# Kernel tuning notes

Hardware: AMD Instinct MI355X
Metric: run time of the kernel (lower is better)

Reference implementation:

```python
import jax, jax.numpy as jnp
import numpy as np

N_WIRES = 8
DIM = 1 << N_WIRES  # 256

# Precompute CNOT permutations (torchquantum convention: wire 0 = MSB)
_idx = np.arange(DIM)
_CNOT_PERMS = []
for _c in range(N_WIRES):
    _t = (_c + 1) % N_WIRES
    _cbit = (_idx >> (N_WIRES - 1 - _c)) & 1
    _CNOT_PERMS.append(np.where(_cbit == 1, _idx ^ (1 << (N_WIRES - 1 - _t)), _idx))
# PauliZ signs per wire: [DIM, N_WIRES]
_ZSIGNS = np.stack([1.0 - 2.0 * ((_idx >> (N_WIRES - 1 - w)) & 1) for w in range(N_WIRES)], axis=1).astype(np.float32)


def _quantum_heads(x, theta):
    """x: [B,S,H,8] angles; theta: [8]. Returns PauliZ expectations [B,S,H,8].

    Simulates per (token,head) an 8-qubit circuit: RX(x_i+theta_i) on wire i
    (encoder RX followed by trainable RX on same wire = one RX with summed angle),
    then CNOT ring 0->1..6->7, 7->0, then MeasureAll PauliZ.
    """
    B, S, H, _ = x.shape
    N = B * S * H
    ang = x.reshape(N, N_WIRES) + theta  # [N,8]
    state = jnp.zeros((N, DIM), dtype=jnp.complex64).at[:, 0].set(1.0)
    half = ang * 0.5
    c_all = jnp.cos(half)
    s_all = jnp.sin(half)
    for w in range(N_WIRES):
        A = 1 << w
        Bdim = 1 << (N_WIRES - 1 - w)
        s = state.reshape(N, A, 2, Bdim)
        a0, a1 = s[:, :, 0, :], s[:, :, 1, :]
        c = c_all[:, w][:, None, None].astype(jnp.complex64)
        isn = (1j * s_all[:, w][:, None, None]).astype(jnp.complex64)
        n0 = c * a0 - isn * a1
        n1 = -isn * a0 + c * a1
        state = jnp.stack([n0, n1], axis=2).reshape(N, DIM)
    for perm in _CNOT_PERMS:
        state = state[:, perm]
    probs = state.real ** 2 + state.imag ** 2  # [N,256]
    exp = probs @ jnp.asarray(_ZSIGNS)  # [N,8]
    return exp.reshape(B, S, H, N_WIRES)


def _mha(proj, W_combine, num_heads):
    # proj: [B,S,E]; q = k = v = proj (identical deterministic projections)
    B, S, E = proj.shape
    d_k = E // num_heads
    qkv = proj.reshape(B, S, num_heads, d_k).transpose(0, 2, 1, 3)  # [B,H,S,dk]
    scores = jnp.einsum('bhqd,bhkd->bhqk', qkv, qkv) / jnp.sqrt(jnp.float32(d_k))
    attn = jax.nn.softmax(scores, axis=-1)
    out = jnp.einsum('bhqk,bhkd->bhqd', attn, qkv)
    out = out.transpose(0, 2, 1, 3).reshape(B, S, E)
    return out @ W_combine.T


def setup_inputs() -> dict:
    key = jax.random.key(0)
    k1, k2, k3 = jax.random.split(key, 3)
    B, S, H = 8, 1024, 8
    E = H * N_WIRES  # 64
    x = jax.random.normal(k1, (B, S, E), dtype=jnp.float32)
    theta = jax.random.normal(k2, (N_WIRES,), dtype=jnp.float32)
    W_combine = jax.random.normal(k3, (E, E), dtype=jnp.float32) * (1.0 / np.sqrt(E))
    return {'x': x, 'theta': theta, 'W_combine': W_combine}


def reference(x, theta, W_combine):
    B, S, E = x.shape
    H = E // N_WIRES
    proj = _quantum_heads(x.reshape(B, S, H, N_WIRES), theta).reshape(B, S, E)
    return _mha(proj, W_combine, H)
```

## Files before the change

### kernel.cpp

```cpp
#include <hip/hip_runtime.h>

typedef _Float16 half4v __attribute__((ext_vector_type(4)));
typedef __fp16 fp16x2 __attribute__((ext_vector_type(2)));
typedef float float4v __attribute__((ext_vector_type(4)));

#define S_ 1024
#define H_ 8
#define B_ 8
#define BH 64
#define NROW 8192
#define E_ 64
#define VST 1032
#define VHALVES (9 * VST)
#define VCHUNK (VHALVES / 8)

static __device__ inline half4v pack4(float a, float b, float c, float d) {
    union { fp16x2 f2[2]; half4v h4; } u;
    u.f2[0] = __builtin_amdgcn_cvt_pkrtz(a, b);
    u.f2[1] = __builtin_amdgcn_cvt_pkrtz(c, d);
    return u.h4;
}

__global__ __launch_bounds__(256) void proj_kernel(
        const float* __restrict__ x, const float* __restrict__ theta,
        _Float16* __restrict__ kG, _Float16* __restrict__ vG) {
    int bh = blockIdx.x >> 2;
    int s  = ((blockIdx.x & 3) << 8) + threadIdx.x;
    int b = bh >> 3, h = bh & 7;

    const float4* xp = (const float4*)(x + (((size_t)(b << 10) + s) << 6) + (h << 3));
    float4 x0 = xp[0];
    float4 x1 = xp[1];
    float c0 = __cosf(x0.x + theta[0]);
    float c1 = __cosf(x0.y + theta[1]);
    float c2 = __cosf(x0.z + theta[2]);
    float c3 = __cosf(x0.w + theta[3]);
    float c4 = __cosf(x1.x + theta[4]);
    float c5 = __cosf(x1.y + theta[5]);
    float c6 = __cosf(x1.z + theta[6]);
    float c7 = __cosf(x1.w + theta[7]);
    float e1 = c0 * c1;
    float e2 = e1 * c2;
    float e3 = e2 * c3;
    float e4 = e3 * c4;
    float e5 = e4 * c5;
    float e6 = e5 * c6;
    float e7 = e6 * c7;
    float e0 = ((c1 * c2) * (c3 * c4)) * ((c5 * c6) * c7);
    half4v lo = pack4(e0, e1, e2, e3);
    half4v hi = pack4(e4, e5, e6, e7);

    _Float16* kgb = kG + (size_t)bh * 8192;
    _Float16* vgb = vG + (size_t)bh * VHALVES;
    int kt = s >> 4, c = s & 15;
    *(half4v*)&kgb[kt * 128 + c * 4]      = lo;
    *(half4v*)&kgb[kt * 128 + 64 + c * 4] = hi;
    vgb[0 * VST + s] = lo[0]; vgb[1 * VST + s] = lo[1];
    vgb[2 * VST + s] = lo[2]; vgb[3 * VST + s] = lo[3];
    vgb[4 * VST + s] = hi[0]; vgb[5 * VST + s] = hi[1];
    vgb[6 * VST + s] = hi[2]; vgb[7 * VST + s] = hi[3];
    if ((blockIdx.x & 3) == 0) {
        const half4v one = {(_Float16)1.f, (_Float16)1.f, (_Float16)1.f, (_Float16)1.f};
        *(half4v*)&vgb[8 * VST + threadIdx.x * 4] = one;
    }
}

__global__ __launch_bounds__(256, 4) void attn_kernel(
        const _Float16* __restrict__ kG, const _Float16* __restrict__ vG,
        _Float16* __restrict__ attnH) {
    __shared__ _Float16 kF[64 * 128];
    __shared__ _Float16 vT[VHALVES];
    int bh = blockIdx.x;
    int b = bh >> 3, h = bh & 7;
    int tid = threadIdx.x;

    {
        const uint4* kg4 = (const uint4*)(kG + (size_t)bh * 8192);
        uint4* kf4 = (uint4*)kF;
#pragma unroll
        for (int i = 0; i < 4; ++i) kf4[tid + i * 256] = kg4[tid + i * 256];
        const uint4* vg4 = (const uint4*)(vG + (size_t)bh * VHALVES);
        uint4* vt4 = (uint4*)vT;
#pragma unroll
        for (int i = 0; i < 4; ++i) vt4[tid + i * 256] = vg4[tid + i * 256];
        if (tid < VCHUNK - 1024) vt4[tid + 1024] = vg4[tid + 1024];
    }
    __syncthreads();

    int lane = tid & 63;
    int wv   = tid >> 6;
    int col  = lane & 15;
    int quad = lane >> 4;
    int q0   = blockIdx.y * 64 + wv * 16;

    bool lo2 = (quad < 2);

    int kbase = (lane & 31) * 4;
    int vcol = (col < 9) ? col : (col - 8);
    int vbase = vcol * VST + quad * 4;

    half4v qf = {(_Float16)0.f, (_Float16)0.f, (_Float16)0.f, (_Float16)0.f};
    if (lo2) qf = *(const half4v*)&kF[kbase + (q0 >> 4) * 128];
    qf *= (_Float16)0.51012921f;

    const float4v zc = {0.f, 0.f, 0.f, 0.f};
    float4v o0 = zc, o1 = zc, o2 = zc, o3 = zc;

#pragma unroll
    for (int kt = 0; kt < 16; ++kt) {
        half4v k0 = *(const half4v*)&kF[kbase + (kt +  0) * 128];
        half4v k1 = *(const half4v*)&kF[kbase + (kt + 16) * 128];
        half4v k2 = *(const half4v*)&kF[kbase + (kt + 32) * 128];
        half4v k3 = *(const half4v*)&kF[kbase + (kt + 48) * 128];
        half4v v0 = *(const half4v*)&vT[vbase + (kt +  0) * 16];
        half4v v1 = *(const half4v*)&vT[vbase + (kt + 16) * 16];
        half4v v2 = *(const half4v*)&vT[vbase + (kt + 32) * 16];
        half4v v3 = *(const half4v*)&vT[vbase + (kt + 48) * 16];
        float4v s0 = __builtin_amdgcn_mfma_f32_16x16x16f16(k0, qf, zc, 0, 0, 0);
        float4v s1 = __builtin_amdgcn_mfma_f32_16x16x16f16(k1, qf, zc, 0, 0, 0);
        float4v s2 = __builtin_amdgcn_mfma_f32_16x16x16f16(k2, qf, zc, 0, 0, 0);
        float4v s3 = __builtin_amdgcn_mfma_f32_16x16x16f16(k3, qf, zc, 0, 0, 0);
        half4v p0 = pack4(__builtin_amdgcn_exp2f(s0[0]), __builtin_amdgcn_exp2f(s0[1]),
                          __builtin_amdgcn_exp2f(s0[2]), __builtin_amdgcn_exp2f(s0[3]));
        half4v p1 = pack4(__builtin_amdgcn_exp2f(s1[0]), __builtin_amdgcn_exp2f(s1[1]),
                          __builtin_amdgcn_exp2f(s1[2]), __builtin_amdgcn_exp2f(s1[3]));
        half4v p2 = pack4(__builtin_amdgcn_exp2f(s2[0]), __builtin_amdgcn_exp2f(s2[1]),
                          __builtin_amdgcn_exp2f(s2[2]), __builtin_amdgcn_exp2f(s2[3]));
        half4v p3 = pack4(__builtin_amdgcn_exp2f(s3[0]), __builtin_amdgcn_exp2f(s3[1]),
                          __builtin_amdgcn_exp2f(s3[2]), __builtin_amdgcn_exp2f(s3[3]));
        o0 = __builtin_amdgcn_mfma_f32_16x16x16f16(v0, p0, o0, 0, 0, 0);
        o1 = __builtin_amdgcn_mfma_f32_16x16x16f16(v1, p1, o1, 0, 0, 0);
        o2 = __builtin_amdgcn_mfma_f32_16x16x16f16(v2, p2, o2, 0, 0, 0);
        o3 = __builtin_amdgcn_mfma_f32_16x16x16f16(v3, p3, o3, 0, 0, 0);
    }

    float4v oacc;
#pragma unroll
    for (int r = 0; r < 4; ++r) oacc[r] = (o0[r] + o1[r]) + (o2[r] + o3[r]);

    float l = __shfl(oacc[0], 32 | col, 64);
    if (lo2) {
        float inv = __builtin_amdgcn_rcpf(l);
        half4v ov = pack4(oacc[0] * inv, oacc[1] * inv, oacc[2] * inv, oacc[3] * inv);
        *(half4v*)(attnH + (((size_t)(b << 10) + q0 + col) << 6) + (h << 3) + quad * 4) = ov;
    }
}

__global__ __launch_bounds__(64) void combine_kernel(
        const _Float16* __restrict__ AH, const float* __restrict__ W,
        float* __restrict__ out) {
    int r0 = blockIdx.x * 16;
    int lane = threadIdx.x;
    int col = lane & 15;
    int quad = lane >> 4;

    half4v af[4];
#pragma unroll
    for (int t = 0; t < 4; ++t)
        af[t] = *(const half4v*)&AH[(size_t)(r0 + col) * 64 + t * 16 + quad * 4];

    float4v acc[4] = {{0,0,0,0},{0,0,0,0},{0,0,0,0},{0,0,0,0}};
#pragma unroll
    for (int e = 0; e < 4; ++e) {
#pragma unroll
        for (int t = 0; t < 4; ++t) {
            float4 w4 = *(const float4*)&W[(size_t)(e * 16 + col) * 64 + t * 16 + quad * 4];
            half4v wf = {(_Float16)w4.x, (_Float16)w4.y, (_Float16)w4.z, (_Float16)w4.w};
            acc[e] = __builtin_amdgcn_mfma_f32_16x16x16f16(af[t], wf, acc[e], 0, 0, 0);
        }
    }

#pragma unroll
    for (int e = 0; e < 4; ++e)
#pragma unroll
        for (int r = 0; r < 4; ++r)
            out[(size_t)(r0 + quad * 4 + r) * E_ + e * 16 + col] = acc[e][r];
}

extern "C" void kernel_launch(void* const* d_in, const int* in_sizes, int n_in,
                              void* d_out, int out_size, void* d_ws, size_t ws_size,
                              hipStream_t stream) {
    const float* x     = (const float*)d_in[0];
    const float* theta = (const float*)d_in[1];
    const float* W     = (const float*)d_in[2];
    float* out = (float*)d_out;

    _Float16* kG    = (_Float16*)d_ws;
    _Float16* vG    = (_Float16*)((char*)d_ws + (2 << 20));
    _Float16* attnH = (_Float16*)((char*)d_ws + (4 << 20));

    proj_kernel<<<BH * 4, 256, 0, stream>>>(x, theta, kG, vG);
    attn_kernel<<<dim3(BH, S_ / 64), 256, 0, stream>>>(kG, vG, attnH);
    combine_kernel<<<NROW / 16, 64, 0, stream>>>(attnH, W, out);
}
```

Measured before the change: 72.31 us.

## Split key range across waves and reduce partial outputs through LDS

Each wave now processes all four query tiles of the block against its own quarter of the keys, rather than one query tile against all keys. Each K and V fragment loaded from LDS is reused across four query MFMAs, which cuts LDS reads per wave by about four times. The four per-wave partial outputs are then summed with an LDS exchange that reuses the K buffer, at the cost of two extra barriers and some reduction traffic.

```diff
diff --git a/kernel.cpp b/kernel.cpp
--- a/kernel.cpp
+++ b/kernel.cpp
@@ -91,35 +91,36 @@
     int wv   = tid >> 6;
     int col  = lane & 15;
     int quad = lane >> 4;
-    int q0   = blockIdx.y * 64 + wv * 16;
-
     bool lo2 = (quad < 2);
 
     int kbase = (lane & 31) * 4;
     int vcol = (col < 9) ? col : (col - 8);
     int vbase = vcol * VST + quad * 4;
-
-    half4v qf = {(_Float16)0.f, (_Float16)0.f, (_Float16)0.f, (_Float16)0.f};
-    if (lo2) qf = *(const half4v*)&kF[kbase + (q0 >> 4) * 128];
-    qf *= (_Float16)0.51012921f;
+    int qt0 = blockIdx.y << 2;
+
+    half4v qf0 = {(_Float16)0.f, (_Float16)0.f, (_Float16)0.f, (_Float16)0.f};
+    half4v qf1 = qf0, qf2 = qf0, qf3 = qf0;
+    if (lo2) {
+        qf0 = *(const half4v*)&kF[kbase + (qt0 + 0) * 128];
+        qf1 = *(const half4v*)&kF[kbase + (qt0 + 1) * 128];
+        qf2 = *(const half4v*)&kF[kbase + (qt0 + 2) * 128];
+        qf3 = *(const half4v*)&kF[kbase + (qt0 + 3) * 128];
+    }
+    const _Float16 qs = (_Float16)0.51012921f;
+    qf0 *= qs; qf1 *= qs; qf2 *= qs; qf3 *= qs;
 
     const float4v zc = {0.f, 0.f, 0.f, 0.f};
     float4v o0 = zc, o1 = zc, o2 = zc, o3 = zc;
 
 #pragma unroll
-    for (int kt = 0; kt < 16; ++kt) {
-        half4v k0 = *(const half4v*)&kF[kbase + (kt +  0) * 128];
-        half4v k1 = *(const half4v*)&kF[kbase + (kt + 16) * 128];
-        half4v k2 = *(const half4v*)&kF[kbase + (kt + 32) * 128];
-        half4v k3 = *(const half4v*)&kF[kbase + (kt + 48) * 128];
-        half4v v0 = *(const half4v*)&vT[vbase + (kt +  0) * 16];
-        half4v v1 = *(const half4v*)&vT[vbase + (kt + 16) * 16];
-        half4v v2 = *(const half4v*)&vT[vbase + (kt + 32) * 16];
-        half4v v3 = *(const half4v*)&vT[vbase + (kt + 48) * 16];
-        float4v s0 = __builtin_amdgcn_mfma_f32_16x16x16f16(k0, qf, zc, 0, 0, 0);
-        float4v s1 = __builtin_amdgcn_mfma_f32_16x16x16f16(k1, qf, zc, 0, 0, 0);
-        float4v s2 = __builtin_amdgcn_mfma_f32_16x16x16f16(k2, qf, zc, 0, 0, 0);
-        float4v s3 = __builtin_amdgcn_mfma_f32_16x16x16f16(k3, qf, zc, 0, 0, 0);
+    for (int i = 0; i < 16; ++i) {
+        int kt = (wv << 4) + i;
+        half4v kf = *(const half4v*)&kF[kbase + kt * 128];
+        half4v vf = *(const half4v*)&vT[vbase + kt * 16];
+        float4v s0 = __builtin_amdgcn_mfma_f32_16x16x16f16(kf, qf0, zc, 0, 0, 0);
+        float4v s1 = __builtin_amdgcn_mfma_f32_16x16x16f16(kf, qf1, zc, 0, 0, 0);
+        float4v s2 = __builtin_amdgcn_mfma_f32_16x16x16f16(kf, qf2, zc, 0, 0, 0);
+        float4v s3 = __builtin_amdgcn_mfma_f32_16x16x16f16(kf, qf3, zc, 0, 0, 0);
         half4v p0 = pack4(__builtin_amdgcn_exp2f(s0[0]), __builtin_amdgcn_exp2f(s0[1]),
                           __builtin_amdgcn_exp2f(s0[2]), __builtin_amdgcn_exp2f(s0[3]));
         half4v p1 = pack4(__builtin_amdgcn_exp2f(s1[0]), __builtin_amdgcn_exp2f(s1[1]),
@@ -128,16 +129,25 @@
                           __builtin_amdgcn_exp2f(s2[2]), __builtin_amdgcn_exp2f(s2[3]));
         half4v p3 = pack4(__builtin_amdgcn_exp2f(s3[0]), __builtin_amdgcn_exp2f(s3[1]),
                           __builtin_amdgcn_exp2f(s3[2]), __builtin_amdgcn_exp2f(s3[3]));
-        o0 = __builtin_amdgcn_mfma_f32_16x16x16f16(v0, p0, o0, 0, 0, 0);
-        o1 = __builtin_amdgcn_mfma_f32_16x16x16f16(v1, p1, o1, 0, 0, 0);
-        o2 = __builtin_amdgcn_mfma_f32_16x16x16f16(v2, p2, o2, 0, 0, 0);
-        o3 = __builtin_amdgcn_mfma_f32_16x16x16f16(v3, p3, o3, 0, 0, 0);
-    }
-
-    float4v oacc;
-#pragma unroll
-    for (int r = 0; r < 4; ++r) oacc[r] = (o0[r] + o1[r]) + (o2[r] + o3[r]);
-
+        o0 = __builtin_amdgcn_mfma_f32_16x16x16f16(vf, p0, o0, 0, 0, 0);
+        o1 = __builtin_amdgcn_mfma_f32_16x16x16f16(vf, p1, o1, 0, 0, 0);
+        o2 = __builtin_amdgcn_mfma_f32_16x16x16f16(vf, p2, o2, 0, 0, 0);
+        o3 = __builtin_amdgcn_mfma_f32_16x16x16f16(vf, p3, o3, 0, 0, 0);
+    }
+
+    __syncthreads();
+    float* red = (float*)kF;
+    *(float4v*)&red[(((wv << 2) + 0) * 64 + lane) << 2] = o0;
+    *(float4v*)&red[(((wv << 2) + 1) * 64 + lane) << 2] = o1;
+    *(float4v*)&red[(((wv << 2) + 2) * 64 + lane) << 2] = o2;
+    *(float4v*)&red[(((wv << 2) + 3) * 64 + lane) << 2] = o3;
+    __syncthreads();
+    float4v oacc = *(const float4v*)&red[((0 * 4 + wv) * 64 + lane) << 2]
+                 + *(const float4v*)&red[((1 * 4 + wv) * 64 + lane) << 2]
+                 + *(const float4v*)&red[((2 * 4 + wv) * 64 + lane) << 2]
+                 + *(const float4v*)&red[((3 * 4 + wv) * 64 + lane) << 2];
+
+    int q0 = (blockIdx.y << 6) + (wv << 4);
     float l = __shfl(oacc[0], 32 | col, 64);
     if (lo2) {
         float inv = __builtin_amdgcn_rcpf(l);
```

New measurement: 72.31 us. Within noise of the previous version (+0.0%).
